# Kernel tuning notes

Measured on AMD Instinct MI355X. Metric: run time of the kernel, lower is better.

Reference implementation:

```python
import jax, jax.numpy as jnp
import numpy as np

KD, KY, KX = 3, 3, 3  # kernel_size from init_kwargs


def setup_inputs() -> dict:
    key = jax.random.key(0)
    x = jax.random.normal(key, (4, 2, 64, 256, 256), dtype=jnp.float32)
    return {"x": x}


def reference(x):
    # x: [B, CH, D, H, W]
    B, CH, D, H, W = x.shape
    pd, py, px = (KD - 1) // 2, (KY - 1) // 2, (KX - 1) // 2
    # replicate padding (torch F.pad mode='replicate' == jnp.pad mode='edge')
    xp = jnp.pad(x, ((0, 0), (0, 0), (pd, pd), (py, py), (px, px)), mode='edge')
    center = (KD * KY * KX) // 2  # flattened center position, excluded from max
    # running max over the 26 non-center neighbors; never materializes the
    # [B, CH, 27, D, H, W] tensor the torch conv3d path creates.
    max_nc = jnp.full(x.shape, -jnp.inf, dtype=x.dtype)
    idx = 0
    for i in range(KD):
        for j in range(KY):
            for k in range(KX):
                if idx != center:
                    shifted = xp[:, :, i:i + D, j:j + H, k:k + W]
                    max_nc = jnp.maximum(max_nc, shifted)
                idx += 1
    mask = x > max_nc  # strict local maximum (excluding self)
    return x * mask.astype(x.dtype)
```

## Files before the change

kernel.cpp:

```cpp
#include <hip/hip_runtime.h>


constexpr int D_   = 64;
constexpr int H_   = 256;
constexpr int W_   = 256;
constexpr int HW_  = H_ * W_;
constexpr int NVOL = 8;
constexpr int DC   = 8;

__device__ __forceinline__ float f3(float a, float b, float c) {
    return fmaxf(fmaxf(a, b), c);
}

__device__ __forceinline__ void dma_row(const float* g, float* l) {
    __builtin_amdgcn_global_load_lds(
        (const __attribute__((address_space(1))) void*)g,
        (__attribute__((address_space(3))) void*)l,
        16, 0, 0);
}

__global__ __launch_bounds__(256, 4)
void nms3d(const float* __restrict__ x, float* __restrict__ out)
{
    __shared__ float buf[4][3][3][W_];

    const int tx = threadIdx.x;
    const int ty = threadIdx.y;
    const int h  = (blockIdx.y << 2) + ty;
    const int n  = blockIdx.z;
    const int z0 = blockIdx.x * DC;
    const int c  = tx << 2;

    const float* __restrict__ base  = x   + (size_t)n * D_ * HW_;
    float* __restrict__       obase = out + (size_t)n * D_ * HW_;

    const int r0 = (h == 0)      ? 0      : h - 1;
    const int r2 = (h == H_ - 1) ? H_ - 1 : h + 1;

    auto stage = [&](int s) {
        const int zc = min(max(z0 - 1 + s, 0), D_ - 1);
        const float* sp = base + (size_t)zc * HW_;
        float* slot = &buf[ty][s % 3][0][0];
        dma_row(sp + r0 * W_ + c, slot);
        dma_row(sp + h  * W_ + c, slot + W_);
        dma_row(sp + r2 * W_ + c, slot + 2 * W_);
    };

    stage(0);
    stage(1);

    float4 vm9_pp = {0,0,0,0};
    float4 vm9_p  = {0,0,0,0};
    float4 cr8_p  = {0,0,0,0};
    float4 vprev  = {0,0,0,0};

#pragma unroll
    for (int t = 0; t < DC + 2; ++t) {
        const int zi = z0 - 1 + t;

        if (t + 2 <= DC + 1) stage(t + 2);

        if      (t <= 2) asm volatile("s_waitcnt vmcnt(6)" ::: "memory");
        else if (t == 3) asm volatile("s_waitcnt vmcnt(7)" ::: "memory");
        else if (t <= 7) asm volatile("s_waitcnt vmcnt(8)" ::: "memory");
        else if (t == 8) asm volatile("s_waitcnt vmcnt(5)" ::: "memory");
        else             asm volatile("s_waitcnt vmcnt(2)" ::: "memory");

        const int sl = t % 3;
        const float4 a = *(const float4*)&buf[ty][sl][0][c];
        const float4 b = *(const float4*)&buf[ty][sl][1][c];
        const float4 d = *(const float4*)&buf[ty][sl][2][c];

        float4 va;
        va.x = fmaxf(a.x, d.x); va.y = fmaxf(a.y, d.y);
        va.z = fmaxf(a.z, d.z); va.w = fmaxf(a.w, d.w);

        float vaL = __shfl_up(va.w, 1);   if (tx == 0)  vaL = va.x;
        float vaR = __shfl_down(va.x, 1); if (tx == 63) vaR = va.w;
        float bL  = __shfl_up(b.w, 1);    if (tx == 0)  bL  = b.x;
        float bR  = __shfl_down(b.x, 1);  if (tx == 63) bR  = b.w;

        float4 hv;
        hv.x = f3(vaL, va.x, va.y);  hv.y = f3(va.x, va.y, va.z);
        hv.z = f3(va.y, va.z, va.w); hv.w = f3(va.z, va.w, vaR);
        float4 nb;
        nb.x = fmaxf(bL, b.y);   nb.y = fmaxf(b.x, b.z);
        nb.z = fmaxf(b.y, b.w);  nb.w = fmaxf(b.z, bR);

        float4 c8, cu;
        c8.x = fmaxf(hv.x, nb.x); c8.y = fmaxf(hv.y, nb.y);
        c8.z = fmaxf(hv.z, nb.z); c8.w = fmaxf(hv.w, nb.w);
        cu.x = fmaxf(c8.x, b.x);  cu.y = fmaxf(c8.y, b.y);
        cu.z = fmaxf(c8.z, b.z);  cu.w = fmaxf(c8.w, b.w);

        if (zi > z0) {
            float4 mx, o;
            mx.x = f3(vm9_pp.x, cr8_p.x, cu.x);
            mx.y = f3(vm9_pp.y, cr8_p.y, cu.y);
            mx.z = f3(vm9_pp.z, cr8_p.z, cu.z);
            mx.w = f3(vm9_pp.w, cr8_p.w, cu.w);
            o.x = vprev.x > mx.x ? vprev.x : 0.0f;
            o.y = vprev.y > mx.y ? vprev.y : 0.0f;
            o.z = vprev.z > mx.z ? vprev.z : 0.0f;
            o.w = vprev.w > mx.w ? vprev.w : 0.0f;
            *(float4*)(obase + (size_t)(zi - 1) * HW_ + (size_t)h * W_ + c) = o;
        }
        vm9_pp = vm9_p; vm9_p = cu; cr8_p = c8; vprev = b;
    }
}

extern "C" void kernel_launch(void* const* d_in, const int* in_sizes, int n_in,
                              void* d_out, int out_size, void* d_ws, size_t ws_size,
                              hipStream_t stream)
{
    const float* x = (const float*)d_in[0];
    float* out = (float*)d_out;
    dim3 block(64, 4, 1);
    dim3 grid(D_ / DC, H_ / 4, NVOL);
    nms3d<<<grid, block, 0, stream>>>(x, out);
}
```

Measured before the change: 232.3 us.

## Process four rows per wave with shared slab and longer depth chunks

Each wave now handles four consecutive output rows from a six-row LDS slab, so each input row is loaded about 1.5 times instead of three times in H. The depth chunk doubles to 16, which cuts the z-halo reloads, and the block shrinks to two waves with a rolled steady-state loop and retuned vmcnt waits. The cost is fewer blocks, more registers per thread for the per-row history, and hand-tuned wait counts that have to match the number of DMA requests in flight.

```diff
diff --git a/kernel.cpp b/kernel.cpp
--- a/kernel.cpp
+++ b/kernel.cpp
@@ -1,12 +1,15 @@
 #include <hip/hip_runtime.h>
 
 
-constexpr int D_   = 64;
-constexpr int H_   = 256;
-constexpr int W_   = 256;
-constexpr int HW_  = H_ * W_;
-constexpr int NVOL = 8;
-constexpr int DC   = 8;
+constexpr int D_    = 64;
+constexpr int H_    = 256;
+constexpr int W_    = 256;
+constexpr int HW_   = H_ * W_;
+constexpr int NVOL  = 8;
+constexpr int DC    = 16;
+constexpr int R_    = 4;
+constexpr int SLAB  = R_ + 2;
+constexpr int WAVES = 2;
 
 __device__ __forceinline__ float f3(float a, float b, float c) {
     return fmaxf(fmaxf(a, b), c);
@@ -19,94 +22,116 @@
         16, 0, 0);
 }
 
-__global__ __launch_bounds__(256, 4)
+__global__ __launch_bounds__(128, 2)
 void nms3d(const float* __restrict__ x, float* __restrict__ out)
 {
-    __shared__ float buf[4][3][3][W_];
+    __shared__ float buf[WAVES][3][SLAB][W_];
 
     const int tx = threadIdx.x;
     const int ty = threadIdx.y;
-    const int h  = (blockIdx.y << 2) + ty;
+    const int h0 = (blockIdx.y * WAVES + ty) * R_;
     const int n  = blockIdx.z;
     const int z0 = blockIdx.x * DC;
     const int c  = tx << 2;
 
-    const float* __restrict__ base  = x   + (size_t)n * D_ * HW_;
-    float* __restrict__       obase = out + (size_t)n * D_ * HW_;
+    const float* __restrict__ base = x   + (size_t)n * D_ * HW_;
+    float* __restrict__       ob   = out + (size_t)n * D_ * HW_;
 
-    const int r0 = (h == 0)      ? 0      : h - 1;
-    const int r2 = (h == H_ - 1) ? H_ - 1 : h + 1;
+    int gj[SLAB];
+#pragma unroll
+    for (int j = 0; j < SLAB; ++j) gj[j] = min(max(h0 - 1 + j, 0), H_ - 1);
 
-    auto stage = [&](int s) {
+    auto stage = [&](int s, int slot) {
         const int zc = min(max(z0 - 1 + s, 0), D_ - 1);
         const float* sp = base + (size_t)zc * HW_;
-        float* slot = &buf[ty][s % 3][0][0];
-        dma_row(sp + r0 * W_ + c, slot);
-        dma_row(sp + h  * W_ + c, slot + W_);
-        dma_row(sp + r2 * W_ + c, slot + 2 * W_);
+        float* sl = &buf[ty][slot][0][0];
+#pragma unroll
+        for (int j = 0; j < SLAB; ++j)
+            dma_row(sp + gj[j] * W_ + c, sl + j * W_);
     };
 
-    stage(0);
-    stage(1);
+    float4 vpp[R_], vp[R_], c8p[R_], vb[R_];
+#pragma unroll
+    for (int i = 0; i < R_; ++i) {
+        vpp[i] = {0,0,0,0}; vp[i] = {0,0,0,0};
+        c8p[i] = {0,0,0,0}; vb[i] = {0,0,0,0};
+    }
 
-    float4 vm9_pp = {0,0,0,0};
-    float4 vm9_p  = {0,0,0,0};
-    float4 cr8_p  = {0,0,0,0};
-    float4 vprev  = {0,0,0,0};
+    auto body = [&](int sl, int zi, bool st) {
+        const float* lp = &buf[ty][sl][0][0];
+        float4 s[SLAB];
+#pragma unroll
+        for (int j = 0; j < SLAB; ++j)
+            s[j] = *(const float4*)(lp + j * W_ + c);
+#pragma unroll
+        for (int i = 0; i < R_; ++i) {
+            const float4 b = s[i + 1];
+            float4 va;
+            va.x = fmaxf(s[i].x, s[i+2].x); va.y = fmaxf(s[i].y, s[i+2].y);
+            va.z = fmaxf(s[i].z, s[i+2].z); va.w = fmaxf(s[i].w, s[i+2].w);
 
-#pragma unroll
-    for (int t = 0; t < DC + 2; ++t) {
-        const int zi = z0 - 1 + t;
+            float vaL = __shfl_up(va.w, 1);   if (tx == 0)  vaL = va.x;
+            float vaR = __shfl_down(va.x, 1); if (tx == 63) vaR = va.w;
+            float bL  = __shfl_up(b.w, 1);    if (tx == 0)  bL  = b.x;
+            float bR  = __shfl_down(b.x, 1);  if (tx == 63) bR  = b.w;
 
-        if (t + 2 <= DC + 1) stage(t + 2);
+            float4 hv, nb, c8, cu;
+            hv.x = f3(vaL, va.x, va.y);  hv.y = f3(va.x, va.y, va.z);
+            hv.z = f3(va.y, va.z, va.w); hv.w = f3(va.z, va.w, vaR);
+            nb.x = fmaxf(bL, b.y);   nb.y = fmaxf(b.x, b.z);
+            nb.z = fmaxf(b.y, b.w);  nb.w = fmaxf(b.z, bR);
+            c8.x = fmaxf(hv.x, nb.x); c8.y = fmaxf(hv.y, nb.y);
+            c8.z = fmaxf(hv.z, nb.z); c8.w = fmaxf(hv.w, nb.w);
+            cu.x = fmaxf(c8.x, b.x);  cu.y = fmaxf(c8.y, b.y);
+            cu.z = fmaxf(c8.z, b.z);  cu.w = fmaxf(c8.w, b.w);
 
-        if      (t <= 2) asm volatile("s_waitcnt vmcnt(6)" ::: "memory");
-        else if (t == 3) asm volatile("s_waitcnt vmcnt(7)" ::: "memory");
-        else if (t <= 7) asm volatile("s_waitcnt vmcnt(8)" ::: "memory");
-        else if (t == 8) asm volatile("s_waitcnt vmcnt(5)" ::: "memory");
-        else             asm volatile("s_waitcnt vmcnt(2)" ::: "memory");
+            if (st) {
+                float4 mx, o;
+                mx.x = f3(vpp[i].x, c8p[i].x, cu.x);
+                mx.y = f3(vpp[i].y, c8p[i].y, cu.y);
+                mx.z = f3(vpp[i].z, c8p[i].z, cu.z);
+                mx.w = f3(vpp[i].w, c8p[i].w, cu.w);
+                o.x = vb[i].x > mx.x ? vb[i].x : 0.0f;
+                o.y = vb[i].y > mx.y ? vb[i].y : 0.0f;
+                o.z = vb[i].z > mx.z ? vb[i].z : 0.0f;
+                o.w = vb[i].w > mx.w ? vb[i].w : 0.0f;
+                *(float4*)(ob + (size_t)(zi - 1) * HW_ + (size_t)(h0 + i) * W_ + c) = o;
+            }
+            vpp[i] = vp[i]; vp[i] = cu; c8p[i] = c8; vb[i] = b;
+        }
+    };
 
-        const int sl = t % 3;
-        const float4 a = *(const float4*)&buf[ty][sl][0][c];
-        const float4 b = *(const float4*)&buf[ty][sl][1][c];
-        const float4 d = *(const float4*)&buf[ty][sl][2][c];
+    stage(0, 0);
+    stage(1, 1);
 
-        float4 va;
-        va.x = fmaxf(a.x, d.x); va.y = fmaxf(a.y, d.y);
-        va.z = fmaxf(a.z, d.z); va.w = fmaxf(a.w, d.w);
+    stage(2, 2);
+    asm volatile("s_waitcnt vmcnt(12)" ::: "memory");
+    body(0, z0 - 1, false);
 
-        float vaL = __shfl_up(va.w, 1);   if (tx == 0)  vaL = va.x;
-        float vaR = __shfl_down(va.x, 1); if (tx == 63) vaR = va.w;
-        float bL  = __shfl_up(b.w, 1);    if (tx == 0)  bL  = b.x;
-        float bR  = __shfl_down(b.x, 1);  if (tx == 63) bR  = b.w;
+    stage(3, 0);
+    asm volatile("s_waitcnt vmcnt(12)" ::: "memory");
+    body(1, z0, false);
 
-        float4 hv;
-        hv.x = f3(vaL, va.x, va.y);  hv.y = f3(va.x, va.y, va.z);
-        hv.z = f3(va.y, va.z, va.w); hv.w = f3(va.z, va.w, vaR);
-        float4 nb;
-        nb.x = fmaxf(bL, b.y);   nb.y = fmaxf(b.x, b.z);
-        nb.z = fmaxf(b.y, b.w);  nb.w = fmaxf(b.z, bR);
+    stage(4, 1);
+    asm volatile("s_waitcnt vmcnt(12)" ::: "memory");
+    body(2, z0 + 1, true);
 
-        float4 c8, cu;
-        c8.x = fmaxf(hv.x, nb.x); c8.y = fmaxf(hv.y, nb.y);
-        c8.z = fmaxf(hv.z, nb.z); c8.w = fmaxf(hv.w, nb.w);
-        cu.x = fmaxf(c8.x, b.x);  cu.y = fmaxf(c8.y, b.y);
-        cu.z = fmaxf(c8.z, b.z);  cu.w = fmaxf(c8.w, b.w);
+    int sl = 0;
+#pragma unroll 1
+    for (int t = 3; t < DC; ++t) {
+        const int slot_stage = (sl + 2) >= 3 ? (sl - 1) : (sl + 2);
+        stage(t + 2, slot_stage);
+        asm volatile("s_waitcnt vmcnt(16)" ::: "memory");
+        body(sl, z0 - 1 + t, true);
+        sl = (sl == 2) ? 0 : sl + 1;
+    }
 
-        if (zi > z0) {
-            float4 mx, o;
-            mx.x = f3(vm9_pp.x, cr8_p.x, cu.x);
-            mx.y = f3(vm9_pp.y, cr8_p.y, cu.y);
-            mx.z = f3(vm9_pp.z, cr8_p.z, cu.z);
-            mx.w = f3(vm9_pp.w, cr8_p.w, cu.w);
-            o.x = vprev.x > mx.x ? vprev.x : 0.0f;
-            o.y = vprev.y > mx.y ? vprev.y : 0.0f;
-            o.z = vprev.z > mx.z ? vprev.z : 0.0f;
-            o.w = vprev.w > mx.w ? vprev.w : 0.0f;
-            *(float4*)(obase + (size_t)(zi - 1) * HW_ + (size_t)h * W_ + c) = o;
-        }
-        vm9_pp = vm9_p; vm9_p = cu; cr8_p = c8; vprev = b;
-    }
+    asm volatile("s_waitcnt vmcnt(14)" ::: "memory");
+    body(sl, z0 - 1 + DC, true);
+    sl = (sl == 2) ? 0 : sl + 1;
+
+    asm volatile("s_waitcnt vmcnt(8)" ::: "memory");
+    body(sl, z0 + DC, true);
 }
 
 extern "C" void kernel_launch(void* const* d_in, const int* in_sizes, int n_in,
@@ -115,7 +140,7 @@
 {
     const float* x = (const float*)d_in[0];
     float* out = (float*)d_out;
-    dim3 block(64, 4, 1);
-    dim3 grid(D_ / DC, H_ / 4, NVOL);
+    dim3 block(64, WAVES, 1);
+    dim3 grid(D_ / DC, H_ / (WAVES * R_), NVOL);
     nms3d<<<grid, block, 0, stream>>>(x, out);
 }
```

New measurement: 246.4 us. 6.0% more time.
